# Optimization experiments

Measured on AMD Instinct MI355X. Metric: run time of the kernel, lower is better.

Reference implementation:

```python
import jax, jax.numpy as jnp
import numpy as np

B, C, W, H = 8, 64, 64, 64
C8 = C // 8


def setup_inputs() -> dict:
    key = jax.random.key(0)
    ks = jax.random.split(key, 8)
    inp = {
        "input": jax.random.normal(ks[0], (B, C, W, H), dtype=jnp.float32),
        "Wf": jax.random.normal(ks[1], (C8, C), dtype=jnp.float32) * (1.0 / np.sqrt(C)),
        "bf": jax.random.normal(ks[2], (C8,), dtype=jnp.float32) * 0.02,
        "Wg": jax.random.normal(ks[3], (C8, C), dtype=jnp.float32) * (1.0 / np.sqrt(C)),
        "bg": jax.random.normal(ks[4], (C8,), dtype=jnp.float32) * 0.02,
        "Wh": jax.random.normal(ks[5], (C, C), dtype=jnp.float32) * (1.0 / np.sqrt(C)),
        "bh": jax.random.normal(ks[6], (C,), dtype=jnp.float32) * 0.02,
        "gamma": jax.random.normal(ks[7], (1,), dtype=jnp.float32) * 0.1,
    }
    return inp


def reference(input, Wf, bf, Wg, bg, Wh, bh, gamma):
    b, c, w, h = input.shape
    n = w * h
    x = input.reshape(b, c, n)                                   # [B,C,N]
    # 1x1 convs == channel matmuls
    f = jnp.einsum('oc,bcn->bon', Wf, x) + bf[None, :, None]     # [B,C/8,N]
    g = jnp.einsum('oc,bcn->bon', Wg, x) + bg[None, :, None]     # [B,C/8,N]
    hh = jnp.einsum('oc,bcn->bon', Wh, x) + bh[None, :, None]    # [B,C,N]
    # s[b,i,j] = sum_k f[b,k,i] * g[b,k,j]  (no 1/sqrt(d) scaling, as in source)
    s = jnp.einsum('bki,bkj->bij', f, g)                         # [B,N,N]
    beta = jax.nn.softmax(s, axis=-1)                            # softmax over j
    # o = bmm(h, beta): o[b,c,i] = sum_j h[b,c,j] * beta[b,j,i]
    o = jnp.einsum('bcj,bji->bci', hh, beta)                     # [B,C,N]
    o = o.reshape(b, c, w, h)
    return gamma * o + input
```

## Files before the change

### kernel.cpp

```cpp
#include <hip/hip_runtime.h>

#define NN 4096
#define LOG2E 1.4426950408889634f

typedef unsigned short u16;
typedef __attribute__((ext_vector_type(8))) short bf16x8;
typedef __attribute__((ext_vector_type(4))) float f32x4;
typedef __attribute__((ext_vector_type(16))) float f32x16;
typedef __attribute__((ext_vector_type(2))) __bf16 bfv2;

__device__ __forceinline__ u16 f2bf(float f){
  union { float f; unsigned u; } v; v.f = f;
  unsigned r = v.u + 0x7fffu + ((v.u >> 16) & 1u);
  return (u16)(r >> 16);
}
__device__ __forceinline__ float bf2f(u16 h){
  union { unsigned u; float f; } v; v.u = ((unsigned)h) << 16;
  return v.f;
}
__device__ __forceinline__ unsigned pk2(float a, float b){
  bfv2 t; t[0] = (__bf16)a; t[1] = (__bf16)b;
  return __builtin_bit_cast(unsigned, t);
}

__global__ __launch_bounds__(512, 4) void prep_kernel(
    const float* __restrict__ x,
    const float* __restrict__ Wf, const float* __restrict__ bfv,
    const float* __restrict__ Wg, const float* __restrict__ bgv,
    const float* __restrict__ Wh, const float* __restrict__ bhv,
    u16* __restrict__ Qg, u16* __restrict__ Kf, u16* __restrict__ V)
{
  __shared__ float xl[64][68];
  const int tid = threadIdx.x;
  const int lane = tid & 63, q8 = tid >> 6;
  const int b = blockIdx.x >> 6;
  const int i0 = (blockIdx.x & 63) << 6;
  const float* xb = x + ((size_t)b << 18);

  for (int r = 0; r < 8; ++r){
    int c = (r << 3) + q8;
    xl[lane][c] = xb[((size_t)c << 12) + i0 + lane];
  }
  __syncthreads();

  float xr[64];
#pragma unroll
  for (int c4 = 0; c4 < 16; ++c4){
    f32x4 v = *(const f32x4*)&xl[lane][c4 << 2];
    xr[c4*4+0]=v[0]; xr[c4*4+1]=v[1]; xr[c4*4+2]=v[2]; xr[c4*4+3]=v[3];
  }

  const int i = i0 + lane;
  const int jh = (i >> 4) & 1;
  const int j16 = i & 15;
  const int sl = (((j16 >> 2) & 1) << 3) + (j16 & 3) + ((j16 >> 3) << 2);
  u16* vp = V + ((size_t)b << 18) + ((size_t)(i >> 5) << 11) + (jh << 10) + sl;
#pragma unroll
  for (int ch = 0; ch < 8; ++ch){
    int co = (q8 << 3) + ch;
    float acc = bhv[co];
    const float* wr = Wh + (co << 6);
#pragma unroll
    for (int c = 0; c < 64; ++c) acc = fmaf(wr[c], xr[c], acc);
    vp[co << 4] = f2bf(acc);
  }
  {
    const int row = (b << 12) + i;
    float a0 = bfv[q8], c0 = bgv[q8];
    const float* w0 = Wf + (q8 << 6);
    const float* u0 = Wg + (q8 << 6);
#pragma unroll
    for (int c = 0; c < 64; ++c){
      float xv = xr[c];
      a0 = fmaf(w0[c], xv, a0);
      c0 = fmaf(u0[c], xv, c0);
    }
    Kf[(size_t)row * 8 + q8] = f2bf(a0 * LOG2E);
    Qg[(size_t)row * 8 + q8] = f2bf(c0);
  }
}

__global__ __launch_bounds__(512, 4) void pass1_kernel(
    const u16* __restrict__ Qg, const u16* __restrict__ Kf, unsigned* __restrict__ Lsp)
{
  __shared__ float zp[8][32];
  const int tid = threadIdx.x;
  const int w = tid >> 6, lane = tid & 63;
  const int l15 = lane & 15, g = lane >> 4;
  const int b = blockIdx.x >> 7;
  const int j0 = (blockIdx.x & 127) << 5;

  bf16x8 af0 = {0,0,0,0,0,0,0,0}, af1 = {0,0,0,0,0,0,0,0};
  if (lane < 16){
    af0 = *(const bf16x8*)(Kf + ((size_t)((b << 12) + j0 + lane)) * 8);
    af1 = *(const bf16x8*)(Kf + ((size_t)((b << 12) + j0 + 16 + lane)) * 8);
  }

  const u16* qb = Qg + ((size_t)(b << 12)) * 8;
  float z[8];
#pragma unroll
  for (int r = 0; r < 8; ++r) z[r] = 0.f;
  const f32x4 zero4 = {0.f,0.f,0.f,0.f};
  const int ibase = w << 9;
  for (int t = 0; t < 16; ++t){
    const int i = ibase + (t << 5);
    bf16x8 b0 = {0,0,0,0,0,0,0,0}, b1 = {0,0,0,0,0,0,0,0};
    if (lane < 16){
      b0 = *(const bf16x8*)(qb + (size_t)(i + lane) * 8);
      b1 = *(const bf16x8*)(qb + (size_t)(i + 16 + lane) * 8);
    }
    f32x4 s00 = __builtin_amdgcn_mfma_f32_16x16x32_bf16(af0, b0, zero4, 0,0,0);
    f32x4 s01 = __builtin_amdgcn_mfma_f32_16x16x32_bf16(af0, b1, zero4, 0,0,0);
    f32x4 s10 = __builtin_amdgcn_mfma_f32_16x16x32_bf16(af1, b0, zero4, 0,0,0);
    f32x4 s11 = __builtin_amdgcn_mfma_f32_16x16x32_bf16(af1, b1, zero4, 0,0,0);
#pragma unroll
    for (int r = 0; r < 4; ++r){
      z[r]     += __builtin_amdgcn_exp2f(s00[r]) + __builtin_amdgcn_exp2f(s01[r]);
      z[4 + r] += __builtin_amdgcn_exp2f(s10[r]) + __builtin_amdgcn_exp2f(s11[r]);
    }
  }
#pragma unroll
  for (int r = 0; r < 8; ++r){
#pragma unroll
    for (int off = 1; off < 16; off <<= 1)
      z[r] += __shfl_xor(z[r], off, 64);
  }
  if (l15 == 0){
#pragma unroll
    for (int r = 0; r < 4; ++r){
      zp[w][(g << 2) + r]      = z[r];
      zp[w][16 + (g << 2) + r] = z[4 + r];
    }
  }
  __syncthreads();
  if (tid < 32){
    float zs = (zp[0][tid] + zp[1][tid]) + (zp[2][tid] + zp[3][tid])
             + (zp[4][tid] + zp[5][tid]) + (zp[6][tid] + zp[7][tid]);
    float nL = -__log2f(zs);
    u16 hi = f2bf(nL);
    u16 lo = f2bf(nL - bf2f(hi));
    Lsp[((size_t)b << 12) + j0 + tid] = (unsigned)hi | ((unsigned)lo << 16);
  }
}

__device__ __forceinline__ bf16x8 pack8(const f32x16 s, const int base){
  union { unsigned d[4]; bf16x8 v; } u;
  u.d[0] = pk2(__builtin_amdgcn_exp2f(s[base+0]), __builtin_amdgcn_exp2f(s[base+1]));
  u.d[1] = pk2(__builtin_amdgcn_exp2f(s[base+2]), __builtin_amdgcn_exp2f(s[base+3]));
  u.d[2] = pk2(__builtin_amdgcn_exp2f(s[base+4]), __builtin_amdgcn_exp2f(s[base+5]));
  u.d[3] = pk2(__builtin_amdgcn_exp2f(s[base+6]), __builtin_amdgcn_exp2f(s[base+7]));
  return u.v;
}

__global__ __launch_bounds__(512, 4) void pass2_kernel(
    const u16* __restrict__ Qg, const u16* __restrict__ Kf,
    const u16* __restrict__ V, const unsigned* __restrict__ Lsp,
    const float* __restrict__ x, const float* __restrict__ gammap,
    float* __restrict__ out)
{
  __shared__ __align__(16) float Of[4][32][68];
  const int tid = threadIdx.x;
  const int w = tid >> 6, lane = tid & 63;
  const int l31 = lane & 31, g2 = lane >> 5;
  const int bid = blockIdx.x;
  const int b = bid & 7;
  const int i0b = (bid >> 3) << 6;

  const u16* kb = Kf + ((size_t)(b << 12)) * 8;
  const u16* vb = V + ((size_t)b << 18);
  const unsigned* Lb = Lsp + ((size_t)b << 12);

  bf16x8 qB0 = {0,0,0,0,0,0,0,0}, qB1 = {0,0,0,0,0,0,0,0};
  if (lane < 32){
    qB0 = *(const bf16x8*)(Qg + ((size_t)((b << 12) + i0b + l31)) * 8);
    qB1 = *(const bf16x8*)(Qg + ((size_t)((b << 12) + i0b + 32 + l31)) * 8);
  } else {
    ((unsigned*)&qB0)[0] = 0x3F803F80u;
    ((unsigned*)&qB1)[0] = 0x3F803F80u;
  }

  f32x16 acc[2][2];
#pragma unroll
  for (int cb = 0; cb < 2; ++cb)
#pragma unroll
    for (int ib = 0; ib < 2; ++ib)
#pragma unroll
      for (int r = 0; r < 16; ++r) acc[cb][ib][r] = 0.f;

  f32x16 zero16;
#pragma unroll
  for (int r = 0; r < 16; ++r) zero16[r] = 0.f;

  const int jbase = w << 9;
  const u16* vlane = vb + (l31 << 4) + (g2 << 3);

  for (int t = 0; t < 16; ++t){
    const int j0 = jbase + (t << 5);
    bf16x8 ka = {0,0,0,0,0,0,0,0};
    if (lane < 32) ka = *(const bf16x8*)(kb + (size_t)(j0 + l31) * 8);
    else ((unsigned*)&ka)[0] = Lb[j0 + l31];
    const u16* vt = vlane + ((size_t)(j0 >> 5) << 11);
    bf16x8 vf00 = *(const bf16x8*)(vt);
    bf16x8 vf10 = *(const bf16x8*)(vt + 512);
    bf16x8 vf01 = *(const bf16x8*)(vt + 1024);
    bf16x8 vf11 = *(const bf16x8*)(vt + 1536);
    f32x16 s0 = __builtin_amdgcn_mfma_f32_32x32x16_bf16(ka, qB0, zero16, 0,0,0);
    f32x16 s1 = __builtin_amdgcn_mfma_f32_32x32x16_bf16(ka, qB1, zero16, 0,0,0);
    bf16x8 p00 = pack8(s0, 0), p01 = pack8(s0, 8);
    bf16x8 p10 = pack8(s1, 0), p11 = pack8(s1, 8);
    __builtin_amdgcn_s_setprio(1);
    acc[0][0] = __builtin_amdgcn_mfma_f32_32x32x16_bf16(vf00, p00, acc[0][0], 0,0,0);
    acc[0][0] = __builtin_amdgcn_mfma_f32_32x32x16_bf16(vf01, p01, acc[0][0], 0,0,0);
    acc[1][0] = __builtin_amdgcn_mfma_f32_32x32x16_bf16(vf10, p00, acc[1][0], 0,0,0);
    acc[1][0] = __builtin_amdgcn_mfma_f32_32x32x16_bf16(vf11, p01, acc[1][0], 0,0,0);
    acc[0][1] = __builtin_amdgcn_mfma_f32_32x32x16_bf16(vf00, p10, acc[0][1], 0,0,0);
    acc[0][1] = __builtin_amdgcn_mfma_f32_32x32x16_bf16(vf01, p11, acc[0][1], 0,0,0);
    acc[1][1] = __builtin_amdgcn_mfma_f32_32x32x16_bf16(vf10, p10, acc[1][1], 0,0,0);
    acc[1][1] = __builtin_amdgcn_mfma_f32_32x32x16_bf16(vf11, p11, acc[1][1], 0,0,0);
    __builtin_amdgcn_s_setprio(0);
  }

  const float gamma = gammap[0];
#pragma unroll
  for (int ib = 0; ib < 2; ++ib){
    if (ib) __syncthreads();
    if (w < 4){
#pragma unroll
      for (int cb = 0; cb < 2; ++cb)
#pragma unroll
        for (int rq = 0; rq < 4; ++rq){
          f32x4 q = { acc[cb][ib][4*rq+0], acc[cb][ib][4*rq+1],
                      acc[cb][ib][4*rq+2], acc[cb][ib][4*rq+3] };
          *(f32x4*)&Of[w][l31][(cb << 5) + (rq << 3) + (g2 << 2)] = q;
        }
    }
    __syncthreads();
    if (w >= 4){
#pragma unroll
      for (int cb = 0; cb < 2; ++cb)
#pragma unroll
        for (int rq = 0; rq < 4; ++rq){
          f32x4 q = { acc[cb][ib][4*rq+0], acc[cb][ib][4*rq+1],
                      acc[cb][ib][4*rq+2], acc[cb][ib][4*rq+3] };
          f32x4* p = (f32x4*)&Of[w - 4][l31][(cb << 5) + (rq << 3) + (g2 << 2)];
          *p += q;
        }
    }
    __syncthreads();
    const int il = tid & 31, cg = tid >> 5;
#pragma unroll
    for (int cc = 0; cc < 4; ++cc){
      const int c = (cg << 2) + cc;
      const size_t idx = (((size_t)((b << 6) + c)) << 12) + i0b + (ib << 5) + il;
      const float o = Of[0][il][c] + Of[1][il][c] + Of[2][il][c] + Of[3][il][c];
      out[idx] = fmaf(gamma, o, x[idx]);
    }
  }
}

extern "C" void kernel_launch(void* const* d_in, const int* in_sizes, int n_in,
                              void* d_out, int out_size, void* d_ws, size_t ws_size,
                              hipStream_t stream)
{
  (void)in_sizes; (void)n_in; (void)out_size; (void)ws_size;
  const float* x   = (const float*)d_in[0];
  const float* Wf  = (const float*)d_in[1];
  const float* bfv = (const float*)d_in[2];
  const float* Wg  = (const float*)d_in[3];
  const float* bgv = (const float*)d_in[4];
  const float* Wh  = (const float*)d_in[5];
  const float* bhv = (const float*)d_in[6];
  const float* gm  = (const float*)d_in[7];
  float* out = (float*)d_out;

  char* ws = (char*)d_ws;
  u16*  Qg = (u16*)(ws);
  u16*  Kf = (u16*)(ws + (1u << 19));
  u16*  Vv = (u16*)(ws + (1u << 20));
  unsigned* Lsp = (unsigned*)(ws + (1u << 20) + (1u << 22));

  prep_kernel<<<512, 512, 0, stream>>>(x, Wf, bfv, Wg, bgv, Wh, bhv, Qg, Kf, Vv);
  pass1_kernel<<<1024, 512, 0, stream>>>(Qg, Kf, Lsp);
  pass2_kernel<<<512, 512, 0, stream>>>(Qg, Kf, Vv, Lsp, x, gm, out);
}
```

Before: 71.85 us.

## Use 32x32 MFMA in pass1 and halve pass2 waves with double-buffered loads

Pass1 now handles 64 key rows per block with 32x32x16 MFMAs instead of 16x16x32, so half as many blocks are launched and each Q fragment load is reused twice. Pass2 drops to 256 threads (4 waves), each wave covering 1024 j values, and software-pipelines the K/V global loads two iterations deep. The epilogue reduction is simplified to two shared-memory slots. This lowers the number of workgroups and the cross-wave reduction overhead and tries to hide load latency. The cost is fewer waves per CU to hide latency and more registers held for the prefetched buffers.

```diff
diff --git a/kernel.cpp b/kernel.cpp
--- a/kernel.cpp
+++ b/kernel.cpp
@@ -83,57 +83,59 @@
 __global__ __launch_bounds__(512, 4) void pass1_kernel(
     const u16* __restrict__ Qg, const u16* __restrict__ Kf, unsigned* __restrict__ Lsp)
 {
-  __shared__ float zp[8][32];
+  __shared__ float zp[8][64];
   const int tid = threadIdx.x;
   const int w = tid >> 6, lane = tid & 63;
-  const int l15 = lane & 15, g = lane >> 4;
-  const int b = blockIdx.x >> 7;
-  const int j0 = (blockIdx.x & 127) << 5;
-
-  bf16x8 af0 = {0,0,0,0,0,0,0,0}, af1 = {0,0,0,0,0,0,0,0};
-  if (lane < 16){
-    af0 = *(const bf16x8*)(Kf + ((size_t)((b << 12) + j0 + lane)) * 8);
-    af1 = *(const bf16x8*)(Kf + ((size_t)((b << 12) + j0 + 16 + lane)) * 8);
+  const int l31 = lane & 31, g2 = lane >> 5;
+  const int bid = blockIdx.x;
+  const int b = bid & 7;
+  const int j0 = ((bid >> 3) & 63) << 6;
+
+  bf16x8 ka0 = {0,0,0,0,0,0,0,0}, ka1 = {0,0,0,0,0,0,0,0};
+  if (lane < 32){
+    ka0 = *(const bf16x8*)(Kf + ((size_t)((b << 12) + j0 + l31)) * 8);
+    ka1 = *(const bf16x8*)(Kf + ((size_t)((b << 12) + j0 + 32 + l31)) * 8);
   }
 
   const u16* qb = Qg + ((size_t)(b << 12)) * 8;
-  float z[8];
-#pragma unroll
-  for (int r = 0; r < 8; ++r) z[r] = 0.f;
-  const f32x4 zero4 = {0.f,0.f,0.f,0.f};
+  f32x16 z0, z1;
+#pragma unroll
+  for (int r = 0; r < 16; ++r){ z0[r] = 0.f; z1[r] = 0.f; }
+  f32x16 zero16;
+#pragma unroll
+  for (int r = 0; r < 16; ++r) zero16[r] = 0.f;
+
   const int ibase = w << 9;
   for (int t = 0; t < 16; ++t){
     const int i = ibase + (t << 5);
-    bf16x8 b0 = {0,0,0,0,0,0,0,0}, b1 = {0,0,0,0,0,0,0,0};
-    if (lane < 16){
-      b0 = *(const bf16x8*)(qb + (size_t)(i + lane) * 8);
-      b1 = *(const bf16x8*)(qb + (size_t)(i + 16 + lane) * 8);
-    }
-    f32x4 s00 = __builtin_amdgcn_mfma_f32_16x16x32_bf16(af0, b0, zero4, 0,0,0);
-    f32x4 s01 = __builtin_amdgcn_mfma_f32_16x16x32_bf16(af0, b1, zero4, 0,0,0);
-    f32x4 s10 = __builtin_amdgcn_mfma_f32_16x16x32_bf16(af1, b0, zero4, 0,0,0);
-    f32x4 s11 = __builtin_amdgcn_mfma_f32_16x16x32_bf16(af1, b1, zero4, 0,0,0);
-#pragma unroll
-    for (int r = 0; r < 4; ++r){
-      z[r]     += __builtin_amdgcn_exp2f(s00[r]) + __builtin_amdgcn_exp2f(s01[r]);
-      z[4 + r] += __builtin_amdgcn_exp2f(s10[r]) + __builtin_amdgcn_exp2f(s11[r]);
-    }
-  }
-#pragma unroll
-  for (int r = 0; r < 8; ++r){
-#pragma unroll
-    for (int off = 1; off < 16; off <<= 1)
-      z[r] += __shfl_xor(z[r], off, 64);
-  }
-  if (l15 == 0){
-#pragma unroll
-    for (int r = 0; r < 4; ++r){
-      zp[w][(g << 2) + r]      = z[r];
-      zp[w][16 + (g << 2) + r] = z[4 + r];
+    bf16x8 qf = {0,0,0,0,0,0,0,0};
+    if (lane < 32) qf = *(const bf16x8*)(qb + (size_t)(i + l31) * 8);
+    f32x16 s0 = __builtin_amdgcn_mfma_f32_32x32x16_bf16(ka0, qf, zero16, 0,0,0);
+    f32x16 s1 = __builtin_amdgcn_mfma_f32_32x32x16_bf16(ka1, qf, zero16, 0,0,0);
+#pragma unroll
+    for (int r = 0; r < 16; ++r){
+      z0[r] += __builtin_amdgcn_exp2f(s0[r]);
+      z1[r] += __builtin_amdgcn_exp2f(s1[r]);
+    }
+  }
+#pragma unroll
+  for (int r = 0; r < 16; ++r){
+#pragma unroll
+    for (int off = 1; off < 32; off <<= 1){
+      z0[r] += __shfl_xor(z0[r], off, 64);
+      z1[r] += __shfl_xor(z1[r], off, 64);
+    }
+  }
+  if (l31 == 0){
+#pragma unroll
+    for (int r = 0; r < 16; ++r){
+      const int jl = (r & 3) + ((r >> 2) << 3) + (g2 << 2);
+      zp[w][jl]      = z0[r];
+      zp[w][32 + jl] = z1[r];
     }
   }
   __syncthreads();
-  if (tid < 32){
+  if (tid < 64){
     float zs = (zp[0][tid] + zp[1][tid]) + (zp[2][tid] + zp[3][tid])
              + (zp[4][tid] + zp[5][tid]) + (zp[6][tid] + zp[7][tid]);
     float nL = -__log2f(zs);
@@ -152,13 +154,13 @@
   return u.v;
 }
 
-__global__ __launch_bounds__(512, 4) void pass2_kernel(
+__global__ __launch_bounds__(256, 2) void pass2_kernel(
     const u16* __restrict__ Qg, const u16* __restrict__ Kf,
     const u16* __restrict__ V, const unsigned* __restrict__ Lsp,
     const float* __restrict__ x, const float* __restrict__ gammap,
     float* __restrict__ out)
 {
-  __shared__ __align__(16) float Of[4][32][68];
+  __shared__ __align__(16) float Of[2][64][68];
   const int tid = threadIdx.x;
   const int w = tid >> 6, lane = tid & 63;
   const int l31 = lane & 31, g2 = lane >> 5;
@@ -179,82 +181,85 @@
     ((unsigned*)&qB1)[0] = 0x3F803F80u;
   }
 
-  f32x16 acc[2][2];
-#pragma unroll
-  for (int cb = 0; cb < 2; ++cb)
-#pragma unroll
-    for (int ib = 0; ib < 2; ++ib)
-#pragma unroll
-      for (int r = 0; r < 16; ++r) acc[cb][ib][r] = 0.f;
-
+  f32x16 acc00, acc01, acc10, acc11;
+#pragma unroll
+  for (int r = 0; r < 16; ++r){ acc00[r]=0.f; acc01[r]=0.f; acc10[r]=0.f; acc11[r]=0.f; }
   f32x16 zero16;
 #pragma unroll
   for (int r = 0; r < 16; ++r) zero16[r] = 0.f;
 
-  const int jbase = w << 9;
+  const int jbase = w << 10;
   const u16* vlane = vb + (l31 << 4) + (g2 << 3);
 
-  for (int t = 0; t < 16; ++t){
-    const int j0 = jbase + (t << 5);
-    bf16x8 ka = {0,0,0,0,0,0,0,0};
+  auto load_all = [&](int tt, bf16x8& ka, bf16x8& v00, bf16x8& v10, bf16x8& v01, bf16x8& v11){
+    const int j0 = jbase + (tt << 5);
+    ka = (bf16x8){0,0,0,0,0,0,0,0};
     if (lane < 32) ka = *(const bf16x8*)(kb + (size_t)(j0 + l31) * 8);
     else ((unsigned*)&ka)[0] = Lb[j0 + l31];
     const u16* vt = vlane + ((size_t)(j0 >> 5) << 11);
-    bf16x8 vf00 = *(const bf16x8*)(vt);
-    bf16x8 vf10 = *(const bf16x8*)(vt + 512);
-    bf16x8 vf01 = *(const bf16x8*)(vt + 1024);
-    bf16x8 vf11 = *(const bf16x8*)(vt + 1536);
-    f32x16 s0 = __builtin_amdgcn_mfma_f32_32x32x16_bf16(ka, qB0, zero16, 0,0,0);
-    f32x16 s1 = __builtin_amdgcn_mfma_f32_32x32x16_bf16(ka, qB1, zero16, 0,0,0);
-    bf16x8 p00 = pack8(s0, 0), p01 = pack8(s0, 8);
-    bf16x8 p10 = pack8(s1, 0), p11 = pack8(s1, 8);
-    __builtin_amdgcn_s_setprio(1);
-    acc[0][0] = __builtin_amdgcn_mfma_f32_32x32x16_bf16(vf00, p00, acc[0][0], 0,0,0);
-    acc[0][0] = __builtin_amdgcn_mfma_f32_32x32x16_bf16(vf01, p01, acc[0][0], 0,0,0);
-    acc[1][0] = __builtin_amdgcn_mfma_f32_32x32x16_bf16(vf10, p00, acc[1][0], 0,0,0);
-    acc[1][0] = __builtin_amdgcn_mfma_f32_32x32x16_bf16(vf11, p01, acc[1][0], 0,0,0);
-    acc[0][1] = __builtin_amdgcn_mfma_f32_32x32x16_bf16(vf00, p10, acc[0][1], 0,0,0);
-    acc[0][1] = __builtin_amdgcn_mfma_f32_32x32x16_bf16(vf01, p11, acc[0][1], 0,0,0);
-    acc[1][1] = __builtin_amdgcn_mfma_f32_32x32x16_bf16(vf10, p10, acc[1][1], 0,0,0);
-    acc[1][1] = __builtin_amdgcn_mfma_f32_32x32x16_bf16(vf11, p11, acc[1][1], 0,0,0);
-    __builtin_amdgcn_s_setprio(0);
-  }
+    v00 = *(const bf16x8*)(vt);
+    v10 = *(const bf16x8*)(vt + 512);
+    v01 = *(const bf16x8*)(vt + 1024);
+    v11 = *(const bf16x8*)(vt + 1536);
+  };
+
+#define COMPUTE(KA, V00, V10, V01, V11)                                              \
+  {                                                                                  \
+    f32x16 s0 = __builtin_amdgcn_mfma_f32_32x32x16_bf16(KA, qB0, zero16, 0,0,0);     \
+    f32x16 s1 = __builtin_amdgcn_mfma_f32_32x32x16_bf16(KA, qB1, zero16, 0,0,0);     \
+    bf16x8 p00 = pack8(s0, 0), p01 = pack8(s0, 8);                                   \
+    bf16x8 p10 = pack8(s1, 0), p11 = pack8(s1, 8);                                   \
+    __builtin_amdgcn_s_setprio(1);                                                   \
+    acc00 = __builtin_amdgcn_mfma_f32_32x32x16_bf16(V00, p00, acc00, 0,0,0);         \
+    acc00 = __builtin_amdgcn_mfma_f32_32x32x16_bf16(V01, p01, acc00, 0,0,0);         \
+    acc10 = __builtin_amdgcn_mfma_f32_32x32x16_bf16(V10, p00, acc10, 0,0,0);         \
+    acc10 = __builtin_amdgcn_mfma_f32_32x32x16_bf16(V11, p01, acc10, 0,0,0);         \
+    acc01 = __builtin_amdgcn_mfma_f32_32x32x16_bf16(V00, p10, acc01, 0,0,0);         \
+    acc01 = __builtin_amdgcn_mfma_f32_32x32x16_bf16(V01, p11, acc01, 0,0,0);         \
+    acc11 = __builtin_amdgcn_mfma_f32_32x32x16_bf16(V10, p10, acc11, 0,0,0);         \
+    acc11 = __builtin_amdgcn_mfma_f32_32x32x16_bf16(V11, p11, acc11, 0,0,0);         \
+    __builtin_amdgcn_s_setprio(0);                                                   \
+  }
+
+  bf16x8 kaA, a00, a10, a01, a11;
+  bf16x8 kaB, b00, b10, b01, b11;
+  load_all(0, kaA, a00, a10, a01, a11);
+
+  for (int t = 0; t < 32; t += 2){
+    load_all(t + 1, kaB, b00, b10, b01, b11);
+    COMPUTE(kaA, a00, a10, a01, a11);
+    if (t + 2 < 32) load_all(t + 2, kaA, a00, a10, a01, a11);
+    COMPUTE(kaB, b00, b10, b01, b11);
+  }
+#undef COMPUTE
 
   const float gamma = gammap[0];
 #pragma unroll
-  for (int ib = 0; ib < 2; ++ib){
-    if (ib) __syncthreads();
-    if (w < 4){
+  for (int pass = 0; pass < 2; ++pass){
+    if ((w >> 1) == pass){
+      const int slot = w & 1;
 #pragma unroll
       for (int cb = 0; cb < 2; ++cb)
 #pragma unroll
-        for (int rq = 0; rq < 4; ++rq){
-          f32x4 q = { acc[cb][ib][4*rq+0], acc[cb][ib][4*rq+1],
-                      acc[cb][ib][4*rq+2], acc[cb][ib][4*rq+3] };
-          *(f32x4*)&Of[w][l31][(cb << 5) + (rq << 3) + (g2 << 2)] = q;
+        for (int ib = 0; ib < 2; ++ib){
+          const f32x16& a = cb ? (ib ? acc11 : acc10) : (ib ? acc01 : acc00);
+#pragma unroll
+          for (int rq = 0; rq < 4; ++rq){
+            f32x4 q = { a[4*rq+0], a[4*rq+1], a[4*rq+2], a[4*rq+3] };
+            f32x4* p = (f32x4*)&Of[slot][(ib << 5) + l31][(cb << 5) + (rq << 3) + (g2 << 2)];
+            if (pass == 0) *p = q; else *p += q;
+          }
         }
     }
     __syncthreads();
-    if (w >= 4){
-#pragma unroll
-      for (int cb = 0; cb < 2; ++cb)
-#pragma unroll
-        for (int rq = 0; rq < 4; ++rq){
-          f32x4 q = { acc[cb][ib][4*rq+0], acc[cb][ib][4*rq+1],
-                      acc[cb][ib][4*rq+2], acc[cb][ib][4*rq+3] };
-          f32x4* p = (f32x4*)&Of[w - 4][l31][(cb << 5) + (rq << 3) + (g2 << 2)];
-          *p += q;
-        }
-    }
-    __syncthreads();
-    const int il = tid & 31, cg = tid >> 5;
-#pragma unroll
-    for (int cc = 0; cc < 4; ++cc){
-      const int c = (cg << 2) + cc;
-      const size_t idx = (((size_t)((b << 6) + c)) << 12) + i0b + (ib << 5) + il;
-      const float o = Of[0][il][c] + Of[1][il][c] + Of[2][il][c] + Of[3][il][c];
-      out[idx] = fmaf(gamma, o, x[idx]);
-    }
+  }
+  const int il = tid & 63, cg = tid >> 6;
+#pragma unroll
+  for (int cc = 0; cc < 16; ++cc){
+    const int c = (cg << 4) + cc;
+    const size_t idx = (((size_t)((b << 6) + c)) << 12) + i0b + il;
+    const float o = Of[0][il][c] + Of[1][il][c];
+    out[idx] = fmaf(gamma, o, x[idx]);
   }
 }
 
@@ -280,6 +285,6 @@
   unsigned* Lsp = (unsigned*)(ws + (1u << 20) + (1u << 22));
 
   prep_kernel<<<512, 512, 0, stream>>>(x, Wf, bfv, Wg, bgv, Wh, bhv, Qg, Kf, Vv);
-  pass1_kernel<<<1024, 512, 0, stream>>>(Qg, Kf, Lsp);
-  pass2_kernel<<<512, 512, 0, stream>>>(Qg, Kf, Vv, Lsp, x, gm, out);
-}
+  pass1_kernel<<<512, 512, 0, stream>>>(Qg, Kf, Lsp);
+  pass2_kernel<<<512, 256, 0, stream>>>(Qg, Kf, Vv, Lsp, x, gm, out);
+}
```

Measured after the change: 67.98 us. -5.4%, faster.
